# Kernel optimization log

Measured on AMD Instinct MI355X. Metric: run time of the kernel, lower is better.

The kernel has to match this reference:

```python
import jax, jax.numpy as jnp
import numpy as np

N_NODES = 50000


def setup_inputs() -> dict:
    key = jax.random.key(0)
    ks = jax.random.split(key, 6)
    L, d = 3, 128
    x = jax.random.normal(ks[0], (N_NODES, d), dtype=jnp.float32)
    edge_index = jax.random.randint(ks[1], (2, 640000), 0, N_NODES, dtype=jnp.int64)
    s = 1.0 / np.sqrt(d)
    W1 = jax.random.normal(ks[2], (L, d, d), dtype=jnp.float32) * s
    W2 = jax.random.normal(ks[3], (L, d, d), dtype=jnp.float32) * s
    b1 = jnp.zeros((L, d), dtype=jnp.float32)
    b2 = jnp.zeros((L, d), dtype=jnp.float32)
    eps = jnp.zeros((L,), dtype=jnp.float32)
    final_w = jax.random.normal(ks[4], (d + L * d, d), dtype=jnp.float32) / np.sqrt(d + L * d)
    final_b = jnp.zeros((d,), dtype=jnp.float32)
    return {"x": x, "edge_index": edge_index, "W1": W1, "b1": b1,
            "W2": W2, "b2": b2, "eps": eps, "final_w": final_w, "final_b": final_b}


def reference(x, edge_index, W1, b1, W2, b2, eps, final_w, final_b):
    src, dst = edge_index[0], edge_index[1]
    num_layers = W1.shape[0]
    xs = [x]
    h = x
    for l in range(num_layers):
        # GINConv: sum-aggregate neighbor features, add (1+eps)*self, then 2-layer MLP
        agg = jax.ops.segment_sum(h[src], dst, num_segments=N_NODES)  # [N, d]
        z = (1.0 + eps[l]) * h + agg
        z = jax.nn.relu(z @ W1[l] + b1[l])
        h = jax.nn.relu(z @ W2[l] + b2[l])
        xs.append(h)
    out = jnp.concatenate(xs, axis=-1)  # [N, in + L*out]
    return out @ final_w + final_b
```

## Files before the change

kernel.cpp:

```cpp
#include <hip/hip_runtime.h>

#define NNODES 50000
#define NEDGES 640000
#define D 128

typedef unsigned short u16;
typedef unsigned int u32;
typedef __bf16 bf16x8 __attribute__((ext_vector_type(8)));
typedef float f32x4 __attribute__((ext_vector_type(4)));
union AB { uint4 u4; bf16x8 f; };

__device__ __forceinline__ u16 f2b(float f) {
    u32 u = __float_as_uint(f);
    return (u16)((u + 0x7fffu + ((u >> 16) & 1u)) >> 16);
}
__device__ __forceinline__ u32 pack2(float lo, float hi) {
    return (u32)f2b(lo) | ((u32)f2b(hi) << 16);
}
__device__ __forceinline__ float blo(u32 v) { return __uint_as_float(v << 16); }
__device__ __forceinline__ float bhi(u32 v) { return __uint_as_float(v & 0xffff0000u); }

__device__ __forceinline__ void acc8(float* a, uint4 v) {
    a[0] += blo(v.x); a[1] += bhi(v.x);
    a[2] += blo(v.y); a[3] += bhi(v.y);
    a[4] += blo(v.z); a[5] += bhi(v.z);
    a[6] += blo(v.w); a[7] += bhi(v.w);
}


__global__ void k_hist(const int* __restrict__ dst, int* __restrict__ cnt) {
    int e = blockIdx.x * 256 + threadIdx.x;
    if (e < NEDGES) atomicAdd(&cnt[dst[e]], 1);
}

__global__ void k_scan1(const int* __restrict__ cnt, int* __restrict__ rp,
                        int* __restrict__ bsum) {
    __shared__ int s[256];
    int tid = threadIdx.x;
    int i = blockIdx.x * 256 + tid;
    int v = (i < NNODES) ? cnt[i] : 0;
    s[tid] = v;
    __syncthreads();
    for (int off = 1; off < 256; off <<= 1) {
        int t = (tid >= off) ? s[tid - off] : 0;
        __syncthreads();
        s[tid] += t;
        __syncthreads();
    }
    if (i < NNODES) rp[i] = s[tid] - v;
    if (tid == 255) bsum[blockIdx.x] = s[255];
}

__global__ void k_scan2(int* __restrict__ bsum, int nb) {
    __shared__ int s[256];
    int tid = threadIdx.x;
    int v = (tid < nb) ? bsum[tid] : 0;
    s[tid] = v;
    __syncthreads();
    for (int off = 1; off < 256; off <<= 1) {
        int t = (tid >= off) ? s[tid - off] : 0;
        __syncthreads();
        s[tid] += t;
        __syncthreads();
    }
    if (tid < nb) bsum[tid] = s[tid] - v;
}

__global__ void k_add(int* __restrict__ rp, const int* __restrict__ bsum) {
    int i = blockIdx.x * 256 + threadIdx.x;
    if (i < NNODES) rp[i] += bsum[blockIdx.x];
    if (i == 0) rp[NNODES] = NEDGES;
}

__global__ void k_scatter(const int* __restrict__ src, const int* __restrict__ dst,
                          const int* __restrict__ rp, int* __restrict__ cnt,
                          int* __restrict__ srcs) {
    int e = blockIdx.x * 256 + threadIdx.x;
    if (e < NEDGES) {
        int dn = dst[e];
        int old = atomicSub(&cnt[dn], 1);
        srcs[rp[dn] + old - 1] = src[e];
    }
}

__global__ void k_prep(const float* __restrict__ W1, const float* __restrict__ W2,
                       const float* __restrict__ fw, const float* __restrict__ x,
                       u16* __restrict__ wT1, u16* __restrict__ wT2,
                       u16* __restrict__ fwTc, u32* __restrict__ xb) {
    int idx = blockIdx.x * 256 + threadIdx.x;
    if (idx < 3 * 16384) {
        int l = idx >> 14, r = idx & 16383, n = r >> 7, k = r & 127;
        wT1[idx] = f2b(W1[l * 16384 + k * 128 + n]);
        wT2[idx] = f2b(W2[l * 16384 + k * 128 + n]);
    }
    if (idx < 4 * 16384) {
        int ch = idx >> 14, r = idx & 16383, n = r >> 7, k = r & 127;
        fwTc[idx] = f2b(fw[(ch * 128 + k) * 128 + n]);
    }
    if (idx < NNODES * 64) {
        float2 v = ((const float2*)x)[idx];
        xb[idx] = pack2(v.x, v.y);
    }
}

template <bool FINAL>
__launch_bounds__(256, 2)
__global__ void k_layer(const uint4* __restrict__ h4, const int* __restrict__ rp,
                        const int* __restrict__ srcs, const float* __restrict__ epsp,
                        const u16* __restrict__ wT1g, const float* __restrict__ b1,
                        const u16* __restrict__ wT2g, const float* __restrict__ b2,
                        u16* __restrict__ H,
                        const u16* __restrict__ xbg, const u16* __restrict__ h1g,
                        const u16* __restrict__ h2g, const u16* __restrict__ fwTc,
                        const float* __restrict__ fb, float* __restrict__ out) {
    __shared__ u16 Tb[128 * 128];
    __shared__ u16 wbuf[128 * 128];
    uint4* Tb4 = (uint4*)Tb;
    uint4* wb4 = (uint4*)wbuf;
    int tid = threadIdx.x;
    int r0 = blockIdx.x * 128;
    int wave = tid >> 6, lane = tid & 63, l16 = lane & 15, quad = lane >> 4;

    {
        const uint4* g = (const uint4*)wT1g;
        for (int i = tid; i < 2048; i += 256) {
            int n = i >> 4, ch = i & 15;
            wb4[n * 16 + ((ch + n) & 15)] = g[i];
        }
    }

    {
        int c = tid & 15;
        int grp = tid >> 4;
        int gbase = lane & 48;
        float sc = 1.0f + epsp[0];
        for (int p = 0; p < 8; ++p) {
            int rloc = p * 16 + grp;
            int node = r0 + rloc;
            uint4 o = make_uint4(0, 0, 0, 0);
            if (node < NNODES) {
                uint4 sv = h4[node * 16 + c];
                float acc[8];
                acc[0] = sc * blo(sv.x); acc[1] = sc * bhi(sv.x);
                acc[2] = sc * blo(sv.y); acc[3] = sc * bhi(sv.y);
                acc[4] = sc * blo(sv.z); acc[5] = sc * bhi(sv.z);
                acc[6] = sc * blo(sv.w); acc[7] = sc * bhi(sv.w);
                int beg = rp[node], end = rp[node + 1];
                for (int base = beg; base < end; base += 16) {
                    int n = end - base; if (n > 16) n = 16;
                    int myidx = (base + c < end) ? srcs[base + c] : 0;
                    int j = 0;
                    for (; j + 8 <= n; j += 8) {
                        int s0 = __shfl(myidx, gbase + j + 0, 64);
                        int s1 = __shfl(myidx, gbase + j + 1, 64);
                        int s2 = __shfl(myidx, gbase + j + 2, 64);
                        int s3 = __shfl(myidx, gbase + j + 3, 64);
                        int s4 = __shfl(myidx, gbase + j + 4, 64);
                        int s5 = __shfl(myidx, gbase + j + 5, 64);
                        int s6 = __shfl(myidx, gbase + j + 6, 64);
                        int s7 = __shfl(myidx, gbase + j + 7, 64);
                        uint4 v0 = h4[s0 * 16 + c]; uint4 v1 = h4[s1 * 16 + c];
                        uint4 v2 = h4[s2 * 16 + c]; uint4 v3 = h4[s3 * 16 + c];
                        uint4 v4 = h4[s4 * 16 + c]; uint4 v5 = h4[s5 * 16 + c];
                        uint4 v6 = h4[s6 * 16 + c]; uint4 v7 = h4[s7 * 16 + c];
                        acc8(acc, v0); acc8(acc, v1); acc8(acc, v2); acc8(acc, v3);
                        acc8(acc, v4); acc8(acc, v5); acc8(acc, v6); acc8(acc, v7);
                    }
                    for (; j + 4 <= n; j += 4) {
                        int s0 = __shfl(myidx, gbase + j + 0, 64);
                        int s1 = __shfl(myidx, gbase + j + 1, 64);
                        int s2 = __shfl(myidx, gbase + j + 2, 64);
                        int s3 = __shfl(myidx, gbase + j + 3, 64);
                        uint4 v0 = h4[s0 * 16 + c]; uint4 v1 = h4[s1 * 16 + c];
                        uint4 v2 = h4[s2 * 16 + c]; uint4 v3 = h4[s3 * 16 + c];
                        acc8(acc, v0); acc8(acc, v1); acc8(acc, v2); acc8(acc, v3);
                    }
                    for (; j < n; ++j) {
                        int s0 = __shfl(myidx, gbase + j, 64);
                        uint4 v0 = h4[s0 * 16 + c];
                        acc8(acc, v0);
                    }
                }
                o.x = pack2(acc[0], acc[1]); o.y = pack2(acc[2], acc[3]);
                o.z = pack2(acc[4], acc[5]); o.w = pack2(acc[6], acc[7]);
            }
            Tb4[rloc * 16 + ((c + rloc) & 15)] = o;
        }
    }
    __syncthreads();

    AB a[2][4];
#pragma unroll
    for (int s = 0; s < 2; ++s) {
        int m = wave * 32 + s * 16 + l16;
#pragma unroll
        for (int kb = 0; kb < 4; ++kb)
            a[s][kb].u4 = Tb4[m * 16 + ((kb * 4 + quad + m) & 15)];
    }
    __syncthreads();

    f32x4 acc[2][8];
#pragma unroll
    for (int col = 0; col < 8; ++col) {
        float bv = b1[col * 16 + l16];
        acc[0][col] = (f32x4){bv, bv, bv, bv};
        acc[1][col] = (f32x4){bv, bv, bv, bv};
    }
#pragma unroll
    for (int col = 0; col < 8; ++col) {
#pragma unroll
        for (int kb = 0; kb < 4; ++kb) {
            AB b;
            int n = col * 16 + l16;
            b.u4 = wb4[n * 16 + ((kb * 4 + quad + n) & 15)];
            acc[0][col] = __builtin_amdgcn_mfma_f32_16x16x32_bf16(a[0][kb].f, b.f, acc[0][col], 0, 0, 0);
            acc[1][col] = __builtin_amdgcn_mfma_f32_16x16x32_bf16(a[1][kb].f, b.f, acc[1][col], 0, 0, 0);
        }
    }

#pragma unroll
    for (int s = 0; s < 2; ++s)
#pragma unroll
        for (int col = 0; col < 8; ++col)
#pragma unroll
            for (int r = 0; r < 4; ++r) {
                int row = wave * 32 + s * 16 + quad * 4 + r;
                int kcol = col * 16 + l16;
                int ch = kcol >> 3;
                Tb[row * 128 + ((ch + row) & 15) * 8 + (kcol & 7)] =
                    f2b(fmaxf(acc[s][col][r], 0.f));
            }
    __syncthreads();

    {
        const uint4* g = (const uint4*)wT2g;
        for (int i = tid; i < 2048; i += 256) {
            int n = i >> 4, ch = i & 15;
            wb4[n * 16 + ((ch + n) & 15)] = g[i];
        }
    }
    AB a2[2][4];
#pragma unroll
    for (int s = 0; s < 2; ++s) {
        int m = wave * 32 + s * 16 + l16;
#pragma unroll
        for (int kb = 0; kb < 4; ++kb)
            a2[s][kb].u4 = Tb4[m * 16 + ((kb * 4 + quad + m) & 15)];
    }
    __syncthreads();

#pragma unroll
    for (int col = 0; col < 8; ++col) {
        float bv = b2[col * 16 + l16];
        acc[0][col] = (f32x4){bv, bv, bv, bv};
        acc[1][col] = (f32x4){bv, bv, bv, bv};
    }
#pragma unroll
    for (int col = 0; col < 8; ++col) {
#pragma unroll
        for (int kb = 0; kb < 4; ++kb) {
            AB b;
            int n = col * 16 + l16;
            b.u4 = wb4[n * 16 + ((kb * 4 + quad + n) & 15)];
            acc[0][col] = __builtin_amdgcn_mfma_f32_16x16x32_bf16(a2[0][kb].f, b.f, acc[0][col], 0, 0, 0);
            acc[1][col] = __builtin_amdgcn_mfma_f32_16x16x32_bf16(a2[1][kb].f, b.f, acc[1][col], 0, 0, 0);
        }
    }

#pragma unroll
    for (int s = 0; s < 2; ++s)
#pragma unroll
        for (int col = 0; col < 8; ++col)
#pragma unroll
            for (int r = 0; r < 4; ++r) {
                int row = wave * 32 + s * 16 + quad * 4 + r;
                int kcol = col * 16 + l16;
                int ch = kcol >> 3;
                Tb[row * 128 + ((ch + row) & 15) * 8 + (kcol & 7)] =
                    f2b(fmaxf(acc[s][col][r], 0.f));
            }

    if constexpr (!FINAL) {
        __syncthreads();
        for (int i = tid; i < 2048; i += 256) {
            int r = i >> 4, ch = i & 15;
            int grow = r0 + r;
            if (grow < NNODES)
                *(uint4*)&H[grow * 128 + ch * 8] = Tb4[r * 16 + ((ch + r) & 15)];
        }
    } else {
#pragma unroll
        for (int col = 0; col < 8; ++col) {
            float bv = fb[col * 16 + l16];
            acc[0][col] = (f32x4){bv, bv, bv, bv};
            acc[1][col] = (f32x4){bv, bv, bv, bv};
        }
        const u16* chin[3] = {xbg, h1g, h2g};
        for (int chn = 0; chn < 4; ++chn) {
            __syncthreads();
            {
                const uint4* g = (const uint4*)(fwTc + chn * 16384);
                for (int i = tid; i < 2048; i += 256) {
                    int n = i >> 4, ch = i & 15;
                    wb4[n * 16 + ((ch + n) & 15)] = g[i];
                }
            }
            AB af[2][4];
            if (chn < 3) {
                const u16* cp = chin[chn];
#pragma unroll
                for (int s = 0; s < 2; ++s) {
                    int row = r0 + wave * 32 + s * 16 + l16;
#pragma unroll
                    for (int kb = 0; kb < 4; ++kb) {
                        if (row < NNODES)
                            af[s][kb].u4 = *(const uint4*)&cp[row * 128 + kb * 32 + quad * 8];
                        else
                            af[s][kb].u4 = make_uint4(0, 0, 0, 0);
                    }
                }
            } else {
#pragma unroll
                for (int s = 0; s < 2; ++s) {
                    int m = wave * 32 + s * 16 + l16;
#pragma unroll
                    for (int kb = 0; kb < 4; ++kb)
                        af[s][kb].u4 = Tb4[m * 16 + ((kb * 4 + quad + m) & 15)];
                }
            }
            __syncthreads();
#pragma unroll
            for (int col = 0; col < 8; ++col) {
#pragma unroll
                for (int kb = 0; kb < 4; ++kb) {
                    AB b;
                    int n = col * 16 + l16;
                    b.u4 = wb4[n * 16 + ((kb * 4 + quad + n) & 15)];
                    acc[0][col] = __builtin_amdgcn_mfma_f32_16x16x32_bf16(af[0][kb].f, b.f, acc[0][col], 0, 0, 0);
                    acc[1][col] = __builtin_amdgcn_mfma_f32_16x16x32_bf16(af[1][kb].f, b.f, acc[1][col], 0, 0, 0);
                }
            }
        }
#pragma unroll
        for (int s = 0; s < 2; ++s)
#pragma unroll
            for (int col = 0; col < 8; ++col)
#pragma unroll
                for (int r = 0; r < 4; ++r) {
                    int row = r0 + wave * 32 + s * 16 + quad * 4 + r;
                    if (row < NNODES) out[row * 128 + col * 16 + l16] = acc[s][col][r];
                }
    }
}

extern "C" void kernel_launch(void* const* d_in, const int* in_sizes, int n_in,
                              void* d_out, int out_size, void* d_ws, size_t ws_size,
                              hipStream_t stream) {
    const float* x   = (const float*)d_in[0];
    const int*   ei  = (const int*)d_in[1];
    const float* W1  = (const float*)d_in[2];
    const float* b1  = (const float*)d_in[3];
    const float* W2  = (const float*)d_in[4];
    const float* b2  = (const float*)d_in[5];
    const float* eps = (const float*)d_in[6];
    const float* fw  = (const float*)d_in[7];
    const float* fb  = (const float*)d_in[8];
    float* out = (float*)d_out;

    const int* srcA = ei;
    const int* dstA = ei + NEDGES;

    char* p = (char*)d_ws;
    size_t off = 0;
    auto take = [&](size_t bytes) {
        char* r = p + off;
        off = (off + bytes + 255) & ~(size_t)255;
        return r;
    };
    int* rp   = (int*)take((NNODES + 1) * sizeof(int));
    int* cnt  = (int*)take(NNODES * sizeof(int));
    int* bsum = (int*)take(256 * sizeof(int));
    int* srcs = (int*)take(NEDGES * sizeof(int));
    u16* wT1  = (u16*)take(3 * 16384 * sizeof(u16));
    u16* wT2  = (u16*)take(3 * 16384 * sizeof(u16));
    u16* fwTc = (u16*)take(4 * 16384 * sizeof(u16));
    u16* xb   = (u16*)take((size_t)NNODES * D * sizeof(u16));
    u16* hb1  = (u16*)take((size_t)NNODES * D * sizeof(u16));
    u16* hb2  = (u16*)take((size_t)NNODES * D * sizeof(u16));
    (void)ws_size; (void)in_sizes; (void)n_in; (void)out_size;

    hipMemsetAsync(cnt, 0, NNODES * sizeof(int), stream);

    int nb = (NNODES + 255) / 256;
    k_hist<<<(NEDGES + 255) / 256, 256, 0, stream>>>(dstA, cnt);
    k_scan1<<<nb, 256, 0, stream>>>(cnt, rp, bsum);
    k_scan2<<<1, 256, 0, stream>>>(bsum, nb);
    k_add<<<nb, 256, 0, stream>>>(rp, bsum);
    k_scatter<<<(NEDGES + 255) / 256, 256, 0, stream>>>(srcA, dstA, rp, cnt, srcs);
    k_prep<<<(NNODES * 64 + 255) / 256, 256, 0, stream>>>(W1, W2, fw, x, wT1, wT2, fwTc, (u32*)xb);

    int gm = (NNODES + 127) / 128;
    k_layer<false><<<gm, 256, 0, stream>>>((const uint4*)xb, rp, srcs, eps + 0,
                                           wT1, b1, wT2, b2, hb1,
                                           nullptr, nullptr, nullptr, nullptr, nullptr, nullptr);
    k_layer<false><<<gm, 256, 0, stream>>>((const uint4*)hb1, rp, srcs, eps + 1,
                                           wT1 + 16384, b1 + D, wT2 + 16384, b2 + D, hb2,
                                           nullptr, nullptr, nullptr, nullptr, nullptr, nullptr);
    k_layer<true><<<gm, 256, 0, stream>>>((const uint4*)hb2, rp, srcs, eps + 2,
                                          wT1 + 2 * 16384, b1 + 2 * D, wT2 + 2 * 16384, b2 + 2 * D,
                                          nullptr,
                                          xb, hb1, hb2, fwTc, fb, out);
}
```

Baseline: 315.8 us.

## Split gather-aggregation from MLP kernel and streamline CSR build

Moves the neighbor sum-aggregation out of the fused layer kernel into a separate high-occupancy k_agg kernel that writes z to a bf16 buffer, and the MLP kernel then reads rows from global memory. CSR construction is simplified: the histogram is folded into the prep kernel and records per-edge slots, a single-block scan replaces three scan kernels, and the scatter needs no atomics. The aim is better latency hiding for the irregular gather, which was limited by the MLP kernel's LDS-bound occupancy, plus fewer launches. In exchange each layer pays an extra write and read of a 50000x128 bf16 buffer, and the scan runs on a single block.

```diff
diff --git a/kernel.cpp b/kernel.cpp
--- a/kernel.cpp
+++ b/kernel.cpp
@@ -27,66 +27,12 @@
     a[6] += blo(v.w); a[7] += bhi(v.w);
 }
 
-
-__global__ void k_hist(const int* __restrict__ dst, int* __restrict__ cnt) {
-    int e = blockIdx.x * 256 + threadIdx.x;
-    if (e < NEDGES) atomicAdd(&cnt[dst[e]], 1);
-}
-
-__global__ void k_scan1(const int* __restrict__ cnt, int* __restrict__ rp,
-                        int* __restrict__ bsum) {
-    __shared__ int s[256];
-    int tid = threadIdx.x;
-    int i = blockIdx.x * 256 + tid;
-    int v = (i < NNODES) ? cnt[i] : 0;
-    s[tid] = v;
-    __syncthreads();
-    for (int off = 1; off < 256; off <<= 1) {
-        int t = (tid >= off) ? s[tid - off] : 0;
-        __syncthreads();
-        s[tid] += t;
-        __syncthreads();
-    }
-    if (i < NNODES) rp[i] = s[tid] - v;
-    if (tid == 255) bsum[blockIdx.x] = s[255];
-}
-
-__global__ void k_scan2(int* __restrict__ bsum, int nb) {
-    __shared__ int s[256];
-    int tid = threadIdx.x;
-    int v = (tid < nb) ? bsum[tid] : 0;
-    s[tid] = v;
-    __syncthreads();
-    for (int off = 1; off < 256; off <<= 1) {
-        int t = (tid >= off) ? s[tid - off] : 0;
-        __syncthreads();
-        s[tid] += t;
-        __syncthreads();
-    }
-    if (tid < nb) bsum[tid] = s[tid] - v;
-}
-
-__global__ void k_add(int* __restrict__ rp, const int* __restrict__ bsum) {
-    int i = blockIdx.x * 256 + threadIdx.x;
-    if (i < NNODES) rp[i] += bsum[blockIdx.x];
-    if (i == 0) rp[NNODES] = NEDGES;
-}
-
-__global__ void k_scatter(const int* __restrict__ src, const int* __restrict__ dst,
-                          const int* __restrict__ rp, int* __restrict__ cnt,
-                          int* __restrict__ srcs) {
-    int e = blockIdx.x * 256 + threadIdx.x;
-    if (e < NEDGES) {
-        int dn = dst[e];
-        int old = atomicSub(&cnt[dn], 1);
-        srcs[rp[dn] + old - 1] = src[e];
-    }
-}
-
 __global__ void k_prep(const float* __restrict__ W1, const float* __restrict__ W2,
                        const float* __restrict__ fw, const float* __restrict__ x,
+                       const int* __restrict__ dst,
                        u16* __restrict__ wT1, u16* __restrict__ wT2,
-                       u16* __restrict__ fwTc, u32* __restrict__ xb) {
+                       u16* __restrict__ fwTc, u32* __restrict__ xb,
+                       int* __restrict__ cnt, int* __restrict__ epos) {
     int idx = blockIdx.x * 256 + threadIdx.x;
     if (idx < 3 * 16384) {
         int l = idx >> 14, r = idx & 16383, n = r >> 7, k = r & 127;
@@ -97,22 +43,115 @@
         int ch = idx >> 14, r = idx & 16383, n = r >> 7, k = r & 127;
         fwTc[idx] = f2b(fw[(ch * 128 + k) * 128 + n]);
     }
+    if (idx < NEDGES) {
+        epos[idx] = atomicAdd(&cnt[dst[idx]], 1);
+    }
     if (idx < NNODES * 64) {
         float2 v = ((const float2*)x)[idx];
         xb[idx] = pack2(v.x, v.y);
     }
 }
 
+__global__ void k_scan(const int* __restrict__ cnt, int* __restrict__ rp) {
+    __shared__ int s[1024];
+    int tid = threadIdx.x;
+    const int IPT = (NNODES + 1023) / 1024;
+    int base = tid * IPT;
+    int sum = 0;
+    for (int i = 0; i < IPT; ++i) {
+        int j = base + i;
+        if (j < NNODES) sum += cnt[j];
+    }
+    s[tid] = sum;
+    __syncthreads();
+    for (int off = 1; off < 1024; off <<= 1) {
+        int t = (tid >= off) ? s[tid - off] : 0;
+        __syncthreads();
+        s[tid] += t;
+        __syncthreads();
+    }
+    int run = s[tid] - sum;
+    for (int i = 0; i < IPT; ++i) {
+        int j = base + i;
+        if (j < NNODES) { rp[j] = run; run += cnt[j]; }
+    }
+    if (tid == 0) rp[NNODES] = NEDGES;
+}
+
+__global__ void k_scatter(const int* __restrict__ src, const int* __restrict__ dst,
+                          const int* __restrict__ rp, const int* __restrict__ epos,
+                          int* __restrict__ srcs) {
+    int e = blockIdx.x * 256 + threadIdx.x;
+    if (e < NEDGES) srcs[rp[dst[e]] + epos[e]] = src[e];
+}
+
+__global__ void k_agg(const uint4* __restrict__ h4, const int* __restrict__ rp,
+                      const int* __restrict__ srcs, const float* __restrict__ epsp,
+                      uint4* __restrict__ z4) {
+    int tid = threadIdx.x;
+    int c = tid & 15;
+    int node = (blockIdx.x * 256 + tid) >> 4;
+    int gbase = tid & 48;
+    float sc = 1.0f + epsp[0];
+
+    uint4 sv = h4[node * 16 + c];
+    float acc[8];
+    acc[0] = sc * blo(sv.x); acc[1] = sc * bhi(sv.x);
+    acc[2] = sc * blo(sv.y); acc[3] = sc * bhi(sv.y);
+    acc[4] = sc * blo(sv.z); acc[5] = sc * bhi(sv.z);
+    acc[6] = sc * blo(sv.w); acc[7] = sc * bhi(sv.w);
+
+    int beg = rp[node], end = rp[node + 1];
+    for (int base = beg; base < end; base += 16) {
+        int n = end - base; if (n > 16) n = 16;
+        int myidx = (base + c < end) ? srcs[base + c] : 0;
+        int j = 0;
+        for (; j + 8 <= n; j += 8) {
+            int s0 = __shfl(myidx, gbase + j + 0, 64);
+            int s1 = __shfl(myidx, gbase + j + 1, 64);
+            int s2 = __shfl(myidx, gbase + j + 2, 64);
+            int s3 = __shfl(myidx, gbase + j + 3, 64);
+            int s4 = __shfl(myidx, gbase + j + 4, 64);
+            int s5 = __shfl(myidx, gbase + j + 5, 64);
+            int s6 = __shfl(myidx, gbase + j + 6, 64);
+            int s7 = __shfl(myidx, gbase + j + 7, 64);
+            uint4 v0 = h4[s0 * 16 + c]; uint4 v1 = h4[s1 * 16 + c];
+            uint4 v2 = h4[s2 * 16 + c]; uint4 v3 = h4[s3 * 16 + c];
+            uint4 v4 = h4[s4 * 16 + c]; uint4 v5 = h4[s5 * 16 + c];
+            uint4 v6 = h4[s6 * 16 + c]; uint4 v7 = h4[s7 * 16 + c];
+            acc8(acc, v0); acc8(acc, v1); acc8(acc, v2); acc8(acc, v3);
+            acc8(acc, v4); acc8(acc, v5); acc8(acc, v6); acc8(acc, v7);
+        }
+        for (; j + 4 <= n; j += 4) {
+            int s0 = __shfl(myidx, gbase + j + 0, 64);
+            int s1 = __shfl(myidx, gbase + j + 1, 64);
+            int s2 = __shfl(myidx, gbase + j + 2, 64);
+            int s3 = __shfl(myidx, gbase + j + 3, 64);
+            uint4 v0 = h4[s0 * 16 + c]; uint4 v1 = h4[s1 * 16 + c];
+            uint4 v2 = h4[s2 * 16 + c]; uint4 v3 = h4[s3 * 16 + c];
+            acc8(acc, v0); acc8(acc, v1); acc8(acc, v2); acc8(acc, v3);
+        }
+        for (; j < n; ++j) {
+            int s0 = __shfl(myidx, gbase + j, 64);
+            uint4 v0 = h4[s0 * 16 + c];
+            acc8(acc, v0);
+        }
+    }
+
+    uint4 o;
+    o.x = pack2(acc[0], acc[1]); o.y = pack2(acc[2], acc[3]);
+    o.z = pack2(acc[4], acc[5]); o.w = pack2(acc[6], acc[7]);
+    z4[node * 16 + c] = o;
+}
+
 template <bool FINAL>
 __launch_bounds__(256, 2)
-__global__ void k_layer(const uint4* __restrict__ h4, const int* __restrict__ rp,
-                        const int* __restrict__ srcs, const float* __restrict__ epsp,
-                        const u16* __restrict__ wT1g, const float* __restrict__ b1,
-                        const u16* __restrict__ wT2g, const float* __restrict__ b2,
-                        u16* __restrict__ H,
-                        const u16* __restrict__ xbg, const u16* __restrict__ h1g,
-                        const u16* __restrict__ h2g, const u16* __restrict__ fwTc,
-                        const float* __restrict__ fb, float* __restrict__ out) {
+__global__ void k_mlp(const u16* __restrict__ A, const u16* __restrict__ wT1g,
+                      const float* __restrict__ b1, const u16* __restrict__ wT2g,
+                      const float* __restrict__ b2, u16* __restrict__ H,
+                      const u16* __restrict__ xbg, const u16* __restrict__ h1g,
+                      const u16* __restrict__ h2g, const u16* __restrict__ fwTc,
+                      const float* __restrict__ fb, float* __restrict__ out) {
     __shared__ u16 Tb[128 * 128];
     __shared__ u16 wbuf[128 * 128];
     uint4* Tb4 = (uint4*)Tb;
@@ -129,73 +168,17 @@
         }
     }
 
-    {
-        int c = tid & 15;
-        int grp = tid >> 4;
-        int gbase = lane & 48;
-        float sc = 1.0f + epsp[0];
-        for (int p = 0; p < 8; ++p) {
-            int rloc = p * 16 + grp;
-            int node = r0 + rloc;
-            uint4 o = make_uint4(0, 0, 0, 0);
-            if (node < NNODES) {
-                uint4 sv = h4[node * 16 + c];
-                float acc[8];
-                acc[0] = sc * blo(sv.x); acc[1] = sc * bhi(sv.x);
-                acc[2] = sc * blo(sv.y); acc[3] = sc * bhi(sv.y);
-                acc[4] = sc * blo(sv.z); acc[5] = sc * bhi(sv.z);
-                acc[6] = sc * blo(sv.w); acc[7] = sc * bhi(sv.w);
-                int beg = rp[node], end = rp[node + 1];
-                for (int base = beg; base < end; base += 16) {
-                    int n = end - base; if (n > 16) n = 16;
-                    int myidx = (base + c < end) ? srcs[base + c] : 0;
-                    int j = 0;
-                    for (; j + 8 <= n; j += 8) {
-                        int s0 = __shfl(myidx, gbase + j + 0, 64);
-                        int s1 = __shfl(myidx, gbase + j + 1, 64);
-                        int s2 = __shfl(myidx, gbase + j + 2, 64);
-                        int s3 = __shfl(myidx, gbase + j + 3, 64);
-                        int s4 = __shfl(myidx, gbase + j + 4, 64);
-                        int s5 = __shfl(myidx, gbase + j + 5, 64);
-                        int s6 = __shfl(myidx, gbase + j + 6, 64);
-                        int s7 = __shfl(myidx, gbase + j + 7, 64);
-                        uint4 v0 = h4[s0 * 16 + c]; uint4 v1 = h4[s1 * 16 + c];
-                        uint4 v2 = h4[s2 * 16 + c]; uint4 v3 = h4[s3 * 16 + c];
-                        uint4 v4 = h4[s4 * 16 + c]; uint4 v5 = h4[s5 * 16 + c];
-                        uint4 v6 = h4[s6 * 16 + c]; uint4 v7 = h4[s7 * 16 + c];
-                        acc8(acc, v0); acc8(acc, v1); acc8(acc, v2); acc8(acc, v3);
-                        acc8(acc, v4); acc8(acc, v5); acc8(acc, v6); acc8(acc, v7);
-                    }
-                    for (; j + 4 <= n; j += 4) {
-                        int s0 = __shfl(myidx, gbase + j + 0, 64);
-                        int s1 = __shfl(myidx, gbase + j + 1, 64);
-                        int s2 = __shfl(myidx, gbase + j + 2, 64);
-                        int s3 = __shfl(myidx, gbase + j + 3, 64);
-                        uint4 v0 = h4[s0 * 16 + c]; uint4 v1 = h4[s1 * 16 + c];
-                        uint4 v2 = h4[s2 * 16 + c]; uint4 v3 = h4[s3 * 16 + c];
-                        acc8(acc, v0); acc8(acc, v1); acc8(acc, v2); acc8(acc, v3);
-                    }
-                    for (; j < n; ++j) {
-                        int s0 = __shfl(myidx, gbase + j, 64);
-                        uint4 v0 = h4[s0 * 16 + c];
-                        acc8(acc, v0);
-                    }
-                }
-                o.x = pack2(acc[0], acc[1]); o.y = pack2(acc[2], acc[3]);
-                o.z = pack2(acc[4], acc[5]); o.w = pack2(acc[6], acc[7]);
-            }
-            Tb4[rloc * 16 + ((c + rloc) & 15)] = o;
-        }
-    }
-    __syncthreads();
-
     AB a[2][4];
 #pragma unroll
     for (int s = 0; s < 2; ++s) {
-        int m = wave * 32 + s * 16 + l16;
-#pragma unroll
-        for (int kb = 0; kb < 4; ++kb)
-            a[s][kb].u4 = Tb4[m * 16 + ((kb * 4 + quad + m) & 15)];
+        int row = r0 + wave * 32 + s * 16 + l16;
+#pragma unroll
+        for (int kb = 0; kb < 4; ++kb) {
+            if (row < NNODES)
+                a[s][kb].u4 = *(const uint4*)&A[row * 128 + kb * 32 + quad * 8];
+            else
+                a[s][kb].u4 = make_uint4(0, 0, 0, 0);
+        }
     }
     __syncthreads();
 
@@ -379,35 +362,34 @@
     };
     int* rp   = (int*)take((NNODES + 1) * sizeof(int));
     int* cnt  = (int*)take(NNODES * sizeof(int));
-    int* bsum = (int*)take(256 * sizeof(int));
+    int* epos = (int*)take(NEDGES * sizeof(int));
     int* srcs = (int*)take(NEDGES * sizeof(int));
     u16* wT1  = (u16*)take(3 * 16384 * sizeof(u16));
     u16* wT2  = (u16*)take(3 * 16384 * sizeof(u16));
     u16* fwTc = (u16*)take(4 * 16384 * sizeof(u16));
     u16* xb   = (u16*)take((size_t)NNODES * D * sizeof(u16));
+    u16* zb   = (u16*)take((size_t)NNODES * D * sizeof(u16));
     u16* hb1  = (u16*)take((size_t)NNODES * D * sizeof(u16));
     u16* hb2  = (u16*)take((size_t)NNODES * D * sizeof(u16));
     (void)ws_size; (void)in_sizes; (void)n_in; (void)out_size;
 
     hipMemsetAsync(cnt, 0, NNODES * sizeof(int), stream);
 
-    int nb = (NNODES + 255) / 256;
-    k_hist<<<(NEDGES + 255) / 256, 256, 0, stream>>>(dstA, cnt);
-    k_scan1<<<nb, 256, 0, stream>>>(cnt, rp, bsum);
-    k_scan2<<<1, 256, 0, stream>>>(bsum, nb);
-    k_add<<<nb, 256, 0, stream>>>(rp, bsum);
-    k_scatter<<<(NEDGES + 255) / 256, 256, 0, stream>>>(srcA, dstA, rp, cnt, srcs);
-    k_prep<<<(NNODES * 64 + 255) / 256, 256, 0, stream>>>(W1, W2, fw, x, wT1, wT2, fwTc, (u32*)xb);
+    k_prep<<<(NNODES * 64 + 255) / 256, 256, 0, stream>>>(W1, W2, fw, x, dstA,
+                                                          wT1, wT2, fwTc, (u32*)xb,
+                                                          cnt, epos);
+    k_scan<<<1, 1024, 0, stream>>>(cnt, rp);
+    k_scatter<<<(NEDGES + 255) / 256, 256, 0, stream>>>(srcA, dstA, rp, epos, srcs);
 
     int gm = (NNODES + 127) / 128;
-    k_layer<false><<<gm, 256, 0, stream>>>((const uint4*)xb, rp, srcs, eps + 0,
-                                           wT1, b1, wT2, b2, hb1,
-                                           nullptr, nullptr, nullptr, nullptr, nullptr, nullptr);
-    k_layer<false><<<gm, 256, 0, stream>>>((const uint4*)hb1, rp, srcs, eps + 1,
-                                           wT1 + 16384, b1 + D, wT2 + 16384, b2 + D, hb2,
-                                           nullptr, nullptr, nullptr, nullptr, nullptr, nullptr);
-    k_layer<true><<<gm, 256, 0, stream>>>((const uint4*)hb2, rp, srcs, eps + 2,
-                                          wT1 + 2 * 16384, b1 + 2 * D, wT2 + 2 * 16384, b2 + 2 * D,
-                                          nullptr,
-                                          xb, hb1, hb2, fwTc, fb, out);
-}
+    k_agg<<<NNODES * 16 / 256, 256, 0, stream>>>((const uint4*)xb, rp, srcs, eps + 0, (uint4*)zb);
+    k_mlp<false><<<gm, 256, 0, stream>>>(zb, wT1, b1, wT2, b2, hb1,
+                                         nullptr, nullptr, nullptr, nullptr, nullptr, nullptr);
+    k_agg<<<NNODES * 16 / 256, 256, 0, stream>>>((const uint4*)hb1, rp, srcs, eps + 1, (uint4*)zb);
+    k_mlp<false><<<gm, 256, 0, stream>>>(zb, wT1 + 16384, b1 + D, wT2 + 16384, b2 + D, hb2,
+                                         nullptr, nullptr, nullptr, nullptr, nullptr, nullptr);
+    k_agg<<<NNODES * 16 / 256, 256, 0, stream>>>((const uint4*)hb2, rp, srcs, eps + 2, (uint4*)zb);
+    k_mlp<true><<<gm, 256, 0, stream>>>(zb, wT1 + 2 * 16384, b1 + 2 * D,
+                                        wT2 + 2 * 16384, b2 + 2 * D, nullptr,
+                                        xb, hb1, hb2, fwTc, fb, out);
+}
```

After: 350.9 us. 11.1% more time.
